# Performance work log

Measured on AMD Instinct MI355X. Metric: run time of the kernel, lower is better.

## Reference

```python
import jax, jax.numpy as jnp
import numpy as np

HID, NH = 2048, 16
QLR, KVLR = 1536, 512
DR, DN, DQK, DV = 64, 128, 192, 128
S = 2048
EPS = 1e-06


def rmsnorm(x, w, eps=EPS):
    return x * jax.lax.rsqrt(jnp.mean(x * x, axis=-1, keepdims=True) + eps) * w


def rope_interleave(x, cos, sin):
    # x: [B,H,S,D]; cos/sin: [B,S,D] (unsqueezed to head dim 1)
    b, h, s, d = x.shape
    # DeepSeek-V3 interleave: (d//2, 2) -> transpose -> flatten
    x = x.reshape(b, h, s, d // 2, 2).swapaxes(3, 4).reshape(b, h, s, d)
    c = cos[:, None, :, :]
    sn = sin[:, None, :, :]
    x1, x2 = x[..., : d // 2], x[..., d // 2:]
    rot = jnp.concatenate([-x2, x1], axis=-1)
    return x * c + rot * sn


def setup_inputs() -> dict:
    key = jax.random.key(0)
    ks = jax.random.split(key, 8)
    hidden_states = jax.random.normal(ks[0], (1, S, HID), dtype=jnp.float32)
    # real RoPE tables for the 64-dim rope part
    inv_freq = 1.0 / (10000.0 ** (np.arange(0, DR, 2, dtype=np.float32) / DR))
    pos = np.arange(S, dtype=np.float32)
    freqs = pos[:, None] * inv_freq[None, :]          # [S, DR/2]
    emb = np.concatenate([freqs, freqs], axis=-1)     # [S, DR]
    cos = jnp.asarray(np.cos(emb), dtype=jnp.float32)[None]
    sin = jnp.asarray(np.sin(emb), dtype=jnp.float32)[None]
    w = 0.02
    wq_a = jax.random.normal(ks[1], (QLR, HID), dtype=jnp.float32) * w
    q_a_ln_w = jnp.ones((QLR,), dtype=jnp.float32)
    wq_b = jax.random.normal(ks[2], (NH * DQK, QLR), dtype=jnp.float32) * w
    wkv_a = jax.random.normal(ks[3], (KVLR + DR, HID), dtype=jnp.float32) * w
    kv_a_ln_w = jnp.ones((KVLR,), dtype=jnp.float32)
    wkv_b = jax.random.normal(ks[4], (NH * (DN + DV), KVLR), dtype=jnp.float32) * w
    wo = jax.random.normal(ks[5], (HID, NH * DV), dtype=jnp.float32) * w
    cu_seqlens = jnp.array([0, S // 2, S], dtype=jnp.int32)  # two packed docs
    return {"hidden_states": hidden_states, "cos": cos, "sin": sin,
            "wq_a": wq_a, "q_a_ln_w": q_a_ln_w, "wq_b": wq_b,
            "wkv_a": wkv_a, "kv_a_ln_w": kv_a_ln_w, "wkv_b": wkv_b,
            "wo": wo, "cu_seqlens": cu_seqlens, "max_seqlen": S // 2}


def reference(hidden_states, cos, sin, wq_a, q_a_ln_w, wq_b, wkv_a, kv_a_ln_w,
              wkv_b, wo, cu_seqlens, max_seqlen):
    B, s, _ = hidden_states.shape
    # LoRA-compressed Q: q_a -> RMSNorm -> q_b
    q = rmsnorm(hidden_states @ wq_a.T, q_a_ln_w) @ wq_b.T       # [B,S,NH*DQK]
    q = q.reshape(B, s, NH, DQK).transpose(0, 2, 1, 3)           # [B,NH,S,DQK]
    q_pass, q_rot = q[..., :DN], q[..., DN:]
    # compressed KV with MQA rope part
    ckv = hidden_states @ wkv_a.T                                 # [B,S,KVLR+DR]
    kv_c, k_rot = ckv[..., :KVLR], ckv[..., KVLR:]
    kv = rmsnorm(kv_c, kv_a_ln_w) @ wkv_b.T                       # [B,S,NH*(DN+DV)]
    kv = kv.reshape(B, s, NH, DN + DV).transpose(0, 2, 1, 3)      # [B,NH,S,DN+DV]
    k_pass, v = kv[..., :DN], kv[..., DN:]
    k_rot = k_rot[:, None, :, :]                                  # [B,1,S,DR]
    q_rot = rope_interleave(q_rot, cos, sin)
    k_rot = rope_interleave(k_rot, cos, sin)
    k_rot = jnp.broadcast_to(k_rot, (B, NH, s, DR))
    qf = jnp.concatenate([q_pass, q_rot], axis=-1)                # [B,NH,S,DQK]
    kf = jnp.concatenate([k_pass, k_rot], axis=-1)                # [B,NH,S,DQK]
    # varlen causal attention: block-diagonal per document + causal
    pos = jnp.arange(s)
    seg = jnp.searchsorted(cu_seqlens[1:], pos, side='right')
    mask = (seg[:, None] == seg[None, :]) & (pos[:, None] >= pos[None, :])
    scale = DQK ** -0.5  # flash default: 1/sqrt(q head dim) (v padded to DQK)
    scores = jnp.einsum('bhqd,bhkd->bhqk', qf, kf) * scale
    scores = jnp.where(mask[None, None], scores, jnp.finfo(scores.dtype).min)
    attn = jax.nn.softmax(scores, axis=-1)
    out = jnp.einsum('bhqk,bhkd->bhqd', attn, v)                  # [B,NH,S,DV]
    out = out.transpose(0, 2, 1, 3).reshape(B, s, NH * DV)
    return out @ wo.T
```

## Files before the change

### kernel.cpp

```cpp
#include <hip/hip_runtime.h>

typedef unsigned short u16;
typedef __attribute__((ext_vector_type(8))) short bf16x8;
typedef __attribute__((ext_vector_type(4))) float f32x4;

#define HID 2048
#define NH 16
#define QLR 1536
#define KVLR 512
#define DR 64
#define DN 128
#define DQK 192
#define DV 128
#define SEQ 2048
#define NKVA 2176
#define SCALE 0.07216878364870323f
#define SCL2 0.1041164359699839f
#define THR2 11.541560327111707f

static __device__ __forceinline__ u16 f2bf(float f) {
  unsigned v = __builtin_bit_cast(unsigned, f);
  v = v + 0x7fffu + ((v >> 16) & 1u);
  return (u16)(v >> 16);
}
static __device__ __forceinline__ float bf2f(u16 u) {
  unsigned v = ((unsigned)u) << 16;
  return __builtin_bit_cast(float, v);
}

#define GLOAD16(gp, lp)                                                        \
  __builtin_amdgcn_global_load_lds(                                            \
      (const __attribute__((address_space(1))) void*)(gp),                     \
      (__attribute__((address_space(3))) void*)(lp), 16, 0, 0)

__global__ void k_convert_all(const float* __restrict__ hs, const float* __restrict__ wq_a,
                              const float* __restrict__ wkv_a, const float* __restrict__ wqb,
                              const float* __restrict__ wkvb, const float* __restrict__ wo,
                              u16* __restrict__ hs_bf, u16* __restrict__ wqkva,
                              u16* __restrict__ wqb_bf, u16* __restrict__ wkvb_bf,
                              u16* __restrict__ wo_bf) {
  const long NQ = 4915200;
  long q = (long)blockIdx.x * blockDim.x + threadIdx.x;
  const long stride = (long)gridDim.x * blockDim.x;
  for (; q < NQ; q += stride) {
    const float* src;
    u16* dst;
    long li;
    bool zero = false;
    if (q < 1048576)        { src = hs;   dst = hs_bf;                      li = q; }
    else if (q < 1835008)   { src = wq_a; dst = wqkva;                      li = q - 1048576; }
    else if (q < 2162688)   { li = q - 1835008; src = wkv_a; dst = wqkva + (size_t)QLR * HID;
                              zero = (li >= 294912); }
    else if (q < 3342336)   { src = wqb;  dst = wqb_bf;                     li = q - 2162688; }
    else if (q < 3866624)   { src = wkvb; dst = wkvb_bf;                    li = q - 3342336; }
    else                    { src = wo;   dst = wo_bf;                      li = q - 3866624; }
    u16 o0 = 0, o1 = 0, o2 = 0, o3 = 0;
    if (!zero) {
      const float4 f = *(const float4*)(src + li * 4);
      o0 = f2bf(f.x); o1 = f2bf(f.y); o2 = f2bf(f.z); o3 = f2bf(f.w);
    }
    u16* d = dst + li * 4;
    d[0] = o0; d[1] = o1; d[2] = o2; d[3] = o3;
  }
}

__global__ void k_rmsnorm2(const float* __restrict__ qkva, const float* __restrict__ qw,
                           const float* __restrict__ kvw, u16* __restrict__ q_ln,
                           u16* __restrict__ kv_ln) {
  const int row = blockIdx.x;
  const int which = blockIdx.y;
  const int t = threadIdx.x;
  const int cols = which ? KVLR : QLR;
  const float inv_cols = which ? (1.0f / KVLR) : (1.0f / QLR);
  const float* x = qkva + (size_t)row * NKVA + (which ? QLR : 0);
  const float* w = which ? kvw : qw;
  u16* Y = (which ? kv_ln : q_ln) + (size_t)row * cols;
  float ss = 0.f;
  for (int i = t * 4; i < cols; i += 1024) {
    float4 v = *(const float4*)(x + i);
    ss += v.x * v.x + v.y * v.y + v.z * v.z + v.w * v.w;
  }
#pragma unroll
  for (int m = 1; m < 64; m <<= 1) ss += __shfl_xor(ss, m, 64);
  __shared__ float red[4];
  if ((t & 63) == 0) red[t >> 6] = ss;
  __syncthreads();
  float tot = red[0] + red[1] + red[2] + red[3];
  float r = rsqrtf(tot * inv_cols + 1e-6f);
  for (int i = t * 4; i < cols; i += 1024) {
    float4 v = *(const float4*)(x + i);
    float4 g = *(const float4*)(w + i);
    u16* y = Y + i;
    y[0] = f2bf(v.x * r * g.x);
    y[1] = f2bf(v.y * r * g.y);
    y[2] = f2bf(v.z * r * g.z);
    y[3] = f2bf(v.w * r * g.w);
  }
}

__global__ __launch_bounds__(256) void k_gemm_nt(
    const u16* __restrict__ A, const u16* __restrict__ B, void* __restrict__ Cout,
    int M, int N, int K, int mode) {
  __shared__ __align__(16) u16 As[2][8192];
  __shared__ __align__(16) u16 Bs[2][8192];
  const int t = threadIdx.x;
  const int lane = t & 63;
  const int w = t >> 6, wr = w >> 1, wc = w & 1;
  const int lm = lane & 15, lg = lane >> 4;

  const int nwg = gridDim.x * gridDim.y;
  int bid = blockIdx.y * gridDim.x + blockIdx.x;
  if ((nwg & 7) == 0) bid = (bid & 7) * (nwg >> 3) + (bid >> 3);
  const int bm = bid % gridDim.y;
  const int bn = bid / gridDim.y;

  const int srow = t >> 3;
  const int scol = ((t & 7) ^ (srow & 7)) * 8;
  const u16* aBase = A + (size_t)(bm * 128 + srow) * K + scol;
  const u16* bBase = B + (size_t)(bn * 128 + srow) * K + scol;
  const size_t rowStep = (size_t)32 * K;

#define STAGE(buf, kt_)                                                        \
  do {                                                                         \
    _Pragma("unroll") for (int p = 0; p < 4; ++p) {                            \
      GLOAD16(aBase + (kt_) + p * rowStep, (u16*)As[buf] + p * 2048 + t * 8);  \
      GLOAD16(bBase + (kt_) + p * rowStep, (u16*)Bs[buf] + p * 2048 + t * 8);  \
    }                                                                          \
  } while (0)

  f32x4 acc[4][4] = {};
  const int nk = K >> 6;
  STAGE(0, 0);
  if (nk > 1) STAGE(1, 64);
  int cur = 0;
  for (int kt = 0; kt < nk; ++kt) {
    if (kt + 1 < nk) asm volatile("s_waitcnt vmcnt(8)" ::: "memory");
    else             asm volatile("s_waitcnt vmcnt(0)" ::: "memory");
    __builtin_amdgcn_s_barrier();
    __builtin_amdgcn_sched_barrier(0);
    bf16x8 af[2][4], bfr[2][4];
#pragma unroll
    for (int kk = 0; kk < 2; ++kk) {
#pragma unroll
      for (int i = 0; i < 4; ++i) {
        const int row_ = wr * 64 + i * 16 + lm;
        af[kk][i] = *(const bf16x8*)(As[cur] + row_ * 64 +
                                     ((((kk << 2) | lg) ^ (row_ & 7)) << 3));
      }
#pragma unroll
      for (int j = 0; j < 4; ++j) {
        const int row_ = wc * 64 + j * 16 + lm;
        bfr[kk][j] = *(const bf16x8*)(Bs[cur] + row_ * 64 +
                                      ((((kk << 2) | lg) ^ (row_ & 7)) << 3));
      }
    }
    asm volatile("s_waitcnt lgkmcnt(0)" ::: "memory");
    __builtin_amdgcn_sched_barrier(0);
    __builtin_amdgcn_s_barrier();
    __builtin_amdgcn_sched_barrier(0);
    if (kt + 2 < nk) STAGE(cur, (kt + 2) << 6);
    __builtin_amdgcn_s_setprio(1);
#pragma unroll
    for (int kk = 0; kk < 2; ++kk)
#pragma unroll
      for (int i = 0; i < 4; ++i)
#pragma unroll
        for (int j = 0; j < 4; ++j)
          acc[i][j] = __builtin_amdgcn_mfma_f32_16x16x32_bf16(af[kk][i], bfr[kk][j],
                                                              acc[i][j], 0, 0, 0);
    __builtin_amdgcn_s_setprio(0);
    cur ^= 1;
  }
#undef STAGE

  const int row0 = bm * 128 + wr * 64 + lg * 4;
  const int col0 = bn * 128 + wc * 64 + lm;
  if (mode == 1) {
    u16* C = (u16*)Cout;
#pragma unroll
    for (int i = 0; i < 4; ++i)
#pragma unroll
      for (int r = 0; r < 4; ++r) {
        u16* crow = C + (size_t)(row0 + i * 16 + r) * N + col0;
#pragma unroll
        for (int j = 0; j < 4; ++j) crow[j * 16] = f2bf(acc[i][j][r]);
      }
  } else {
    float* C = (float*)Cout;
#pragma unroll
    for (int i = 0; i < 4; ++i)
#pragma unroll
      for (int r = 0; r < 4; ++r) {
        float* crow = C + (size_t)(row0 + i * 16 + r) * N + col0;
#pragma unroll
        for (int j = 0; j < 4; ++j) crow[j * 16] = acc[i][j][r];
      }
  }
}

template <int WN>
__global__ __launch_bounds__(512) void k_gemm_nt8(
    const u16* __restrict__ A, const u16* __restrict__ B, void* __restrict__ Cout,
    int M, int N, int K, int mode) {
  constexpr int BN = WN * 64;
  constexpr int NST = 2 + WN;
  __shared__ __align__(16) u16 As[3][128 * 64];
  __shared__ __align__(16) u16 Bs[3][BN * 64];
  const int t = threadIdx.x;
  const int lane = t & 63;
  const int w = t >> 6, wr = w >> 2, wc = w & 3;
  const int lm = lane & 15, lg = lane >> 4;

  const int nwg = gridDim.x * gridDim.y;
  int bid = blockIdx.y * gridDim.x + blockIdx.x;
  if ((nwg & 7) == 0) bid = (bid & 7) * (nwg >> 3) + (bid >> 3);
  const int bm = bid % gridDim.y;
  const int bn = bid / gridDim.y;

  const u16* aT = A + (size_t)bm * 128 * K;
  const u16* bT = B + (size_t)bn * BN * K;

#define STAGE8(buf, kt_)                                                       \
  do {                                                                         \
    _Pragma("unroll") for (int i = 0; i < 2; ++i) {                            \
      const int g = t + i * 512, row = g >> 3, slot = (g & 7) ^ (row & 7);     \
      GLOAD16(aT + (size_t)row * K + slot * 8 + (kt_), (u16*)As[buf] + g * 8); \
    }                                                                          \
    _Pragma("unroll") for (int i = 0; i < WN; ++i) {                           \
      const int g = t + i * 512, row = g >> 3, slot = (g & 7) ^ (row & 7);     \
      GLOAD16(bT + (size_t)row * K + slot * 8 + (kt_), (u16*)Bs[buf] + g * 8); \
    }                                                                          \
  } while (0)

  f32x4 acc[4][WN] = {};
  const int nk = K >> 6;
  STAGE8(0, 0);
  if (nk > 1) STAGE8(1, 64);
  if (nk > 2) STAGE8(2, 128);
  int bt = 0;
  for (int kt = 0; kt < nk; ++kt) {
    const int rem = nk - 1 - kt;
    if (rem >= 2)      asm volatile("s_waitcnt vmcnt(%0)" :: "i"(2 * NST) : "memory");
    else if (rem == 1) asm volatile("s_waitcnt vmcnt(%0)" :: "i"(NST) : "memory");
    else               asm volatile("s_waitcnt vmcnt(0)" ::: "memory");
    __builtin_amdgcn_s_barrier();
    __builtin_amdgcn_sched_barrier(0);
    bf16x8 af[2][4], bfr[2][WN];
#pragma unroll
    for (int kk = 0; kk < 2; ++kk) {
#pragma unroll
      for (int i = 0; i < 4; ++i) {
        const int row_ = wr * 64 + i * 16 + lm;
        af[kk][i] = *(const bf16x8*)(As[bt] + row_ * 64 +
                                     ((((kk << 2) | lg) ^ (row_ & 7)) << 3));
      }
#pragma unroll
      for (int j = 0; j < WN; ++j) {
        const int row_ = wc * (WN * 16) + j * 16 + lm;
        bfr[kk][j] = *(const bf16x8*)(Bs[bt] + row_ * 64 +
                                      ((((kk << 2) | lg) ^ (row_ & 7)) << 3));
      }
    }
    asm volatile("s_waitcnt lgkmcnt(0)" ::: "memory");
    __builtin_amdgcn_sched_barrier(0);
    __builtin_amdgcn_s_barrier();
    __builtin_amdgcn_sched_barrier(0);
    if (kt + 3 < nk) STAGE8(bt, (kt + 3) << 6);
    __builtin_amdgcn_s_setprio(1);
#pragma unroll
    for (int kk = 0; kk < 2; ++kk)
#pragma unroll
      for (int i = 0; i < 4; ++i)
#pragma unroll
        for (int j = 0; j < WN; ++j)
          acc[i][j] = __builtin_amdgcn_mfma_f32_16x16x32_bf16(af[kk][i], bfr[kk][j],
                                                              acc[i][j], 0, 0, 0);
    __builtin_amdgcn_s_setprio(0);
    bt = (bt == 2) ? 0 : bt + 1;
  }
#undef STAGE8

  const int row0 = bm * 128 + wr * 64 + lg * 4;
  const int col0 = bn * BN + wc * (WN * 16) + lm;
  if (mode == 1) {
    u16* C = (u16*)Cout;
#pragma unroll
    for (int i = 0; i < 4; ++i)
#pragma unroll
      for (int r = 0; r < 4; ++r) {
        u16* crow = C + (size_t)(row0 + i * 16 + r) * N + col0;
#pragma unroll
        for (int j = 0; j < WN; ++j) crow[j * 16] = f2bf(acc[i][j][r]);
      }
  } else {
    float* C = (float*)Cout;
#pragma unroll
    for (int i = 0; i < 4; ++i)
#pragma unroll
      for (int r = 0; r < 4; ++r) {
        float* crow = C + (size_t)(row0 + i * 16 + r) * N + col0;
#pragma unroll
        for (int j = 0; j < WN; ++j) crow[j * 16] = acc[i][j][r];
      }
  }
}

__global__ __launch_bounds__(256) void k_mk_all(
    const u16* __restrict__ qfull, const u16* __restrict__ kvfull,
    const float* __restrict__ krot, int krot_stride,
    const float* __restrict__ cosb, const float* __restrict__ sinb,
    u16* __restrict__ qf, u16* __restrict__ kf, u16* __restrict__ vt) {
  __shared__ u16 vts[128][66];
  const int s0 = blockIdx.x * 64, h = blockIdx.y, t = threadIdx.x;
#pragma unroll
  for (int i = 0; i < 8; ++i) {
    const int g = t + i * 256, row = g >> 5, slot = g & 31;
    const u16* src = kvfull + (size_t)(s0 + row) * (NH * 256) + h * 256 + slot * 8;
    bf16x8 v = *(const bf16x8*)src;
    if (slot < 16) {
      *(bf16x8*)(kf + ((size_t)h * SEQ + s0 + row) * DQK + slot * 8) = v;
    } else {
      const int d = (slot - 16) * 8;
#pragma unroll
      for (int e = 0; e < 8; ++e) vts[d + e][row] = (u16)v[e];
    }
  }
#pragma unroll
  for (int i = 0; i < 8; ++i) {
    const int g = t + i * 256, row = g >> 5, c = g & 31;
    float a = krot[(size_t)(s0 + row) * krot_stride + 2 * c];
    float b = krot[(size_t)(s0 + row) * krot_stride + 2 * c + 1];
    float cc = cosb[(size_t)(s0 + row) * DR + c];
    float sn = sinb[(size_t)(s0 + row) * DR + c];
    u16* kd = kf + ((size_t)h * SEQ + s0 + row) * DQK;
    kd[DN + c] = f2bf(a * cc - b * sn);
    kd[DN + 32 + c] = f2bf(b * cc + a * sn);
  }
  __syncthreads();
#pragma unroll
  for (int i = 0; i < 4; ++i) {
    const int g = t + i * 256, d = g >> 3, slot = g & 7;
    bf16x8 v;
#pragma unroll
    for (int e = 0; e < 8; ++e) v[e] = (short)vts[d][slot * 8 + e];
    *(bf16x8*)(vt + ((size_t)h * DV + d) * SEQ + s0 + slot * 8) = v;
  }
#pragma unroll
  for (int i = 0; i < 4; ++i) {
    const int g = t + i * 256, row = g >> 4, vc = g & 15;
    const u16* src = qfull + (size_t)(s0 + row) * (NH * DQK) + h * DQK + vc * 8;
    bf16x8 v = *(const bf16x8*)src;
    bf16x8 o;
#pragma unroll
    for (int e = 0; e < 8; ++e) o[e] = (short)f2bf(bf2f((u16)v[e]) * SCL2);
    *(bf16x8*)(qf + ((size_t)h * SEQ + s0 + row) * DQK + vc * 8) = o;
  }
#pragma unroll
  for (int i = 0; i < 8; ++i) {
    const int g = t + i * 256, row = g >> 5, c = g & 31;
    const u16* src = qfull + (size_t)(s0 + row) * (NH * DQK) + h * DQK;
    float a = bf2f(src[DN + 2 * c]);
    float b = bf2f(src[DN + 2 * c + 1]);
    float cc = cosb[(size_t)(s0 + row) * DR + c];
    float sn = sinb[(size_t)(s0 + row) * DR + c];
    u16* qd = qf + ((size_t)h * SEQ + s0 + row) * DQK;
    qd[DN + c] = f2bf((a * cc - b * sn) * SCL2);
    qd[DN + 32 + c] = f2bf((b * cc + a * sn) * SCL2);
  }
}

__global__ __launch_bounds__(256) void k_attn(
    const u16* __restrict__ qf, const u16* __restrict__ kf, const u16* __restrict__ vt,
    u16* __restrict__ attn_out) {
  __shared__ __align__(16) u16 Ks[3][32 * 192];
  __shared__ __align__(16) u16 Vs[3][128 * 32];
  __shared__ __align__(16) u16 p_lds[4][16][32];

  const int t = threadIdx.x, lane = t & 63, w = t >> 6;
  const int lm = lane & 15, lg = lane >> 4;
  const int bid = blockIdx.x;
  const int x = bid & 7, rr = bid >> 3;
  const int i5 = rr & 31, late = rr >> 5;
  const int tj = late ? (i5 >> 2) : 15 - (i5 >> 2);
  const int h = x * 2 + ((i5 >> 1) & 1);
  const int seg = i5 & 1;
  const int tile_row0 = seg * 1024 + tj * 64;
  const int k_begin = seg * 1024;
  const int n_kt = tj * 2 + 2;

  const int lo_row = tile_row0 + w * 16;
  bf16x8 qfr[6];
  {
    const u16* qp = qf + ((size_t)h * SEQ + (lo_row + lm)) * DQK + lg * 8;
#pragma unroll
    for (int c = 0; c < 6; ++c) qfr[c] = *(const bf16x8*)(qp + c * 32);
  }
  int qrow[4];
#pragma unroll
  for (int r = 0; r < 4; ++r) qrow[r] = lo_row + lg * 4 + r;

  float m_r[4], l_loc[4];
#pragma unroll
  for (int r = 0; r < 4; ++r) { m_r[r] = -3.0e4f; l_loc[r] = 0.f; }
  f32x4 oacc[8] = {};
  bf16x8 pa, vv[8];

#define STAGE(buf, kt_)                                                        \
  do {                                                                         \
    const int k0_ = k_begin + (kt_) * 32;                                      \
    _Pragma("unroll") for (int p = 0; p < 3; ++p) {                            \
      const int id = p * 256 + t;                                              \
      const int row = id / 24, colL = id - row * 24;                           \
      const u16* g = kf + ((size_t)h * SEQ + k0_ + row) * DQK +                \
                     ((colL ^ (row & 7)) * 8);                                 \
      GLOAD16(g, (u16*)Ks[buf] + id * 8);                                      \
    }                                                                          \
    _Pragma("unroll") for (int p = 0; p < 2; ++p) {                            \
      const int id = p * 256 + t;                                              \
      const int row = id >> 2, colL = id & 3;                                  \
      const u16* g = vt + ((size_t)h * DV + row) * SEQ + k0_ +                 \
                     ((colL ^ (row & 3)) * 8);                                 \
      GLOAD16(g, (u16*)Vs[buf] + id * 8);                                      \
    }                                                                          \
  } while (0)

#define COMPUTE1(buf, kt_)                                                     \
  do {                                                                         \
    const int k0_ = k_begin + (kt_) * 32;                                      \
    f32x4 sc[2] = {};                                                          \
    __builtin_amdgcn_s_setprio(1);                                             \
    _Pragma("unroll") for (int n0_ = 0; n0_ < 2; ++n0_)                        \
        _Pragma("unroll") for (int c_ = 0; c_ < 6; ++c_) {                     \
      const int row_ = n0_ * 16 + lm, cc_ = c_ * 4 + lg;                       \
      bf16x8 kfr = *(const bf16x8*)(Ks[buf] + row_ * 192 +                     \
                                    ((cc_ ^ (row_ & 7)) * 8));                 \
      sc[n0_] = __builtin_amdgcn_mfma_f32_16x16x32_bf16(qfr[c_], kfr,          \
                                                        sc[n0_], 0, 0, 0);     \
    }                                                                          \
    __builtin_amdgcn_s_setprio(0);                                             \
    _Pragma("unroll") for (int nd = 0; nd < 8; ++nd) {   \
      const int row_ = nd * 16 + lm;                      \
      vv[nd] = *(const bf16x8*)(Vs[buf] + row_ * 32 +                          \
                                ((lg ^ (row_ & 3)) * 8));                      \
    }                                                                          \
    float s0a[4], s1a[4];                                                      \
    float over = -1e30f;                                                       \
    if (lo_row >= k0_ + 31) {                                                  \
      _Pragma("unroll") for (int r = 0; r < 4; ++r) {                          \
        s0a[r] = sc[0][r];                                                     \
        s1a[r] = sc[1][r];                                                     \
        over = fmaxf(over, fmaxf(s0a[r], s1a[r]) - m_r[r]);                    \
      }                                                                        \
    } else {                                                                   \
      const int kc0 = k0_ + lm, kc1 = k0_ + 16 + lm;                           \
      _Pragma("unroll") for (int r = 0; r < 4; ++r) {                          \
        s0a[r] = (kc0 <= qrow[r]) ? sc[0][r] : -1e30f;                         \
        s1a[r] = (kc1 <= qrow[r]) ? sc[1][r] : -1e30f;                         \
        over = fmaxf(over, fmaxf(s0a[r], s1a[r]) - m_r[r]);                    \
      }                                                                        \
    }                                                                          \
    if (__any(over > THR2)) {                                                  \
      _Pragma("unroll") for (int r = 0; r < 4; ++r) {                          \
        float mx = fmaxf(s0a[r], s1a[r]);                                      \
        _Pragma("unroll") for (int md = 1; md < 16; md <<= 1)                  \
            mx = fmaxf(mx, __shfl_xor(mx, md, 64));                            \
        float mnew = fmaxf(m_r[r], mx);                                        \
        float alpha = exp2f(m_r[r] - mnew);                                    \
        m_r[r] = mnew;                                                         \
        l_loc[r] *= alpha;                                                     \
        _Pragma("unroll") for (int nd = 0; nd < 8; ++nd) oacc[nd][r] *= alpha; \
      }                                                                        \
    }                                                                          \
    _Pragma("unroll") for (int r = 0; r < 4; ++r) {                            \
      float p0 = exp2f(s0a[r] - m_r[r]);                                       \
      float p1 = exp2f(s1a[r] - m_r[r]);                                       \
      l_loc[r] += p0 + p1;                                                     \
      p_lds[w][lg * 4 + r][lm] = f2bf(p0);                                     \
      p_lds[w][lg * 4 + r][16 + lm] = f2bf(p1);                                \
    }                                                                          \
    asm volatile("s_waitcnt lgkmcnt(0)" ::: "memory");                         \
    __builtin_amdgcn_sched_barrier(0);                                         \
    pa = *(const bf16x8*)(&p_lds[w][lm][lg * 8]);                              \
  } while (0)

  STAGE(0, 0);
  STAGE(1, 1);
  if (n_kt > 2) STAGE(2, 2);
  int bt = 0;
  for (int kt = 0; kt < n_kt; ++kt) {
    const int rem = n_kt - 1 - kt;
    if (rem >= 2)      asm volatile("s_waitcnt vmcnt(10)" ::: "memory");
    else if (rem == 1) asm volatile("s_waitcnt vmcnt(5)" ::: "memory");
    else               asm volatile("s_waitcnt vmcnt(0)" ::: "memory");
    __builtin_amdgcn_s_barrier();
    __builtin_amdgcn_sched_barrier(0);
    COMPUTE1(bt, kt);
    asm volatile("s_waitcnt lgkmcnt(0)" ::: "memory");
    __builtin_amdgcn_sched_barrier(0);
    __builtin_amdgcn_s_barrier();
    __builtin_amdgcn_sched_barrier(0);
    if (kt + 3 < n_kt) STAGE(bt, kt + 3);
    __builtin_amdgcn_s_setprio(1);
#pragma unroll
    for (int nd = 0; nd < 8; ++nd)
      oacc[nd] = __builtin_amdgcn_mfma_f32_16x16x32_bf16(pa, vv[nd], oacc[nd], 0, 0, 0);
    __builtin_amdgcn_s_setprio(0);
    bt = (bt == 2) ? 0 : bt + 1;
  }
#undef STAGE
#undef COMPUTE1

#pragma unroll
  for (int r = 0; r < 4; ++r) {
    float lt = l_loc[r];
#pragma unroll
    for (int md = 1; md < 16; md <<= 1) lt += __shfl_xor(lt, md, 64);
    float inv = 1.0f / lt;
#pragma unroll
    for (int nd = 0; nd < 8; ++nd)
      attn_out[(size_t)qrow[r] * (NH * DV) + h * DV + nd * 16 + lm] =
          f2bf(oacc[nd][r] * inv);
  }
}

extern "C" void kernel_launch(void* const* d_in, const int* in_sizes, int n_in,
                              void* d_out, int out_size, void* d_ws, size_t ws_size,
                              hipStream_t stream) {
  const float* hs = (const float*)d_in[0];
  const float* cosb = (const float*)d_in[1];
  const float* sinb = (const float*)d_in[2];
  const float* wq_a = (const float*)d_in[3];
  const float* q_a_ln_w = (const float*)d_in[4];
  const float* wq_b = (const float*)d_in[5];
  const float* wkv_a = (const float*)d_in[6];
  const float* kv_a_ln_w = (const float*)d_in[7];
  const float* wkv_b = (const float*)d_in[8];
  const float* wo = (const float*)d_in[9];

  char* ws = (char*)d_ws;
  size_t off = 0;
  auto take = [&](size_t bytes) {
    size_t o = off;
    off += (bytes + 255) & ~(size_t)255;
    return o;
  };
  u16* hs_bf = (u16*)(ws + take((size_t)SEQ * HID * 2));
  u16* wqkva = (u16*)(ws + take((size_t)NKVA * HID * 2));
  u16* wqb = (u16*)(ws + take((size_t)(NH * DQK) * QLR * 2));
  u16* wkvb = (u16*)(ws + take((size_t)(NH * 256) * KVLR * 2));
  u16* wo_bf = (u16*)(ws + take((size_t)HID * (NH * DV) * 2));
  float* qkva = (float*)(ws + take((size_t)SEQ * NKVA * 4));
  u16* q_ln = (u16*)(ws + take((size_t)SEQ * QLR * 2));
  u16* kv_ln = (u16*)(ws + take((size_t)SEQ * KVLR * 2));
  u16* qfull = (u16*)(ws + take((size_t)SEQ * NH * DQK * 2));
  u16* kvfull = (u16*)(ws + take((size_t)SEQ * NH * 256 * 2));
  u16* qf = (u16*)(ws + take((size_t)NH * SEQ * DQK * 2));
  u16* kf = (u16*)(ws + take((size_t)NH * SEQ * DQK * 2));
  u16* vt = (u16*)(ws + take((size_t)NH * DV * SEQ * 2));
  u16* attn = (u16*)(ws + take((size_t)SEQ * NH * DV * 2));
  if (off > ws_size) return;

  k_convert_all<<<2048, 256, 0, stream>>>(hs, wq_a, wkv_a, wq_b, wkv_b, wo,
                                          hs_bf, wqkva, wqb, wkvb, wo_bf);

  dim3 g1(NKVA / 128, SEQ / 128);
  k_gemm_nt8<2><<<g1, 512, 0, stream>>>(hs_bf, wqkva, qkva, SEQ, NKVA, HID, 0);

  k_rmsnorm2<<<dim3(SEQ, 2), 256, 0, stream>>>(qkva, q_a_ln_w, kv_a_ln_w, q_ln, kv_ln);

  dim3 g2(NH * DQK / 192, SEQ / 128);
  k_gemm_nt8<3><<<g2, 512, 0, stream>>>(q_ln, wqb, qfull, SEQ, NH * DQK, QLR, 1);
  dim3 g3(NH * 256 / 256, SEQ / 128);
  k_gemm_nt8<4><<<g3, 512, 0, stream>>>(kv_ln, wkvb, kvfull, SEQ, NH * 256, KVLR, 1);

  k_mk_all<<<dim3(SEQ / 64, NH), 256, 0, stream>>>(qfull, kvfull, qkva + (QLR + KVLR),
                                                   NKVA, cosb, sinb, qf, kf, vt);

  k_attn<<<512, 256, 0, stream>>>(qf, kf, vt, attn);

  dim3 g4(HID / 128, SEQ / 128);
  k_gemm_nt<<<g4, 256, 0, stream>>>(attn, wo_bf, d_out, SEQ, HID, NH * DV, 0);
}
```

Measured before the change: 201.6 us.

## Split-K the first projection GEMM and fold partial sums into consumers

The q_a/kv_a projection GEMM now runs as a two-way split-K using the 256-thread kernel with a z grid dimension. Each half writes its own fp32 partial buffer, and the RMSNorm and k_rot/RoPE kernels add the two partials when they load them, so no separate reduction kernel is needed. The output projection switches to the 512-thread nt8 kernel with WN=2. This aims to fill more CUs on the small 17x16 tile grid, at the cost of an extra fp32 write and read of the SEQxNKVA intermediate.

New measurement: 187.9 us. -6.8%, faster.

```diff
diff --git a/kernel.cpp b/kernel.cpp
--- a/kernel.cpp
+++ b/kernel.cpp
@@ -64,21 +64,25 @@
   }
 }
 
-__global__ void k_rmsnorm2(const float* __restrict__ qkva, const float* __restrict__ qw,
-                           const float* __restrict__ kvw, u16* __restrict__ q_ln,
-                           u16* __restrict__ kv_ln) {
+__global__ void k_rmsnorm2(const float* __restrict__ qkva0, const float* __restrict__ qkva1,
+                           const float* __restrict__ qw, const float* __restrict__ kvw,
+                           u16* __restrict__ q_ln, u16* __restrict__ kv_ln) {
   const int row = blockIdx.x;
   const int which = blockIdx.y;
   const int t = threadIdx.x;
   const int cols = which ? KVLR : QLR;
   const float inv_cols = which ? (1.0f / KVLR) : (1.0f / QLR);
-  const float* x = qkva + (size_t)row * NKVA + (which ? QLR : 0);
+  const size_t base = (size_t)row * NKVA + (which ? QLR : 0);
+  const float* x0 = qkva0 + base;
+  const float* x1 = qkva1 + base;
   const float* w = which ? kvw : qw;
   u16* Y = (which ? kv_ln : q_ln) + (size_t)row * cols;
   float ss = 0.f;
   for (int i = t * 4; i < cols; i += 1024) {
-    float4 v = *(const float4*)(x + i);
-    ss += v.x * v.x + v.y * v.y + v.z * v.z + v.w * v.w;
+    float4 a = *(const float4*)(x0 + i);
+    float4 b = *(const float4*)(x1 + i);
+    float vx = a.x + b.x, vy = a.y + b.y, vz = a.z + b.z, vw = a.w + b.w;
+    ss += vx * vx + vy * vy + vz * vz + vw * vw;
   }
 #pragma unroll
   for (int m = 1; m < 64; m <<= 1) ss += __shfl_xor(ss, m, 64);
@@ -88,19 +92,20 @@
   float tot = red[0] + red[1] + red[2] + red[3];
   float r = rsqrtf(tot * inv_cols + 1e-6f);
   for (int i = t * 4; i < cols; i += 1024) {
-    float4 v = *(const float4*)(x + i);
+    float4 a = *(const float4*)(x0 + i);
+    float4 b = *(const float4*)(x1 + i);
     float4 g = *(const float4*)(w + i);
     u16* y = Y + i;
-    y[0] = f2bf(v.x * r * g.x);
-    y[1] = f2bf(v.y * r * g.y);
-    y[2] = f2bf(v.z * r * g.z);
-    y[3] = f2bf(v.w * r * g.w);
+    y[0] = f2bf((a.x + b.x) * r * g.x);
+    y[1] = f2bf((a.y + b.y) * r * g.y);
+    y[2] = f2bf((a.z + b.z) * r * g.z);
+    y[3] = f2bf((a.w + b.w) * r * g.w);
   }
 }
 
 __global__ __launch_bounds__(256) void k_gemm_nt(
-    const u16* __restrict__ A, const u16* __restrict__ B, void* __restrict__ Cout,
-    int M, int N, int K, int mode) {
+    const u16* __restrict__ A, const u16* __restrict__ B, float* __restrict__ Cout,
+    int M, int N, int K, int klen) {
   __shared__ __align__(16) u16 As[2][8192];
   __shared__ __align__(16) u16 Bs[2][8192];
   const int t = threadIdx.x;
@@ -113,11 +118,12 @@
   if ((nwg & 7) == 0) bid = (bid & 7) * (nwg >> 3) + (bid >> 3);
   const int bm = bid % gridDim.y;
   const int bn = bid / gridDim.y;
+  const int k0 = blockIdx.z * klen;
 
   const int srow = t >> 3;
   const int scol = ((t & 7) ^ (srow & 7)) * 8;
-  const u16* aBase = A + (size_t)(bm * 128 + srow) * K + scol;
-  const u16* bBase = B + (size_t)(bn * 128 + srow) * K + scol;
+  const u16* aBase = A + (size_t)(bm * 128 + srow) * K + scol + k0;
+  const u16* bBase = B + (size_t)(bn * 128 + srow) * K + scol + k0;
   const size_t rowStep = (size_t)32 * K;
 
 #define STAGE(buf, kt_)                                                        \
@@ -129,7 +135,7 @@
   } while (0)
 
   f32x4 acc[4][4] = {};
-  const int nk = K >> 6;
+  const int nk = klen >> 6;
   STAGE(0, 0);
   if (nk > 1) STAGE(1, 64);
   int cur = 0;
@@ -175,27 +181,15 @@
 
   const int row0 = bm * 128 + wr * 64 + lg * 4;
   const int col0 = bn * 128 + wc * 64 + lm;
-  if (mode == 1) {
-    u16* C = (u16*)Cout;
-#pragma unroll
-    for (int i = 0; i < 4; ++i)
-#pragma unroll
-      for (int r = 0; r < 4; ++r) {
-        u16* crow = C + (size_t)(row0 + i * 16 + r) * N + col0;
-#pragma unroll
-        for (int j = 0; j < 4; ++j) crow[j * 16] = f2bf(acc[i][j][r]);
-      }
-  } else {
-    float* C = (float*)Cout;
-#pragma unroll
-    for (int i = 0; i < 4; ++i)
-#pragma unroll
-      for (int r = 0; r < 4; ++r) {
-        float* crow = C + (size_t)(row0 + i * 16 + r) * N + col0;
-#pragma unroll
-        for (int j = 0; j < 4; ++j) crow[j * 16] = acc[i][j][r];
-      }
-  }
+  float* C = Cout + (size_t)blockIdx.z * M * N;
+#pragma unroll
+  for (int i = 0; i < 4; ++i)
+#pragma unroll
+    for (int r = 0; r < 4; ++r) {
+      float* crow = C + (size_t)(row0 + i * 16 + r) * N + col0;
+#pragma unroll
+      for (int j = 0; j < 4; ++j) crow[j * 16] = acc[i][j][r];
+    }
 }
 
 template <int WN>
@@ -307,7 +301,7 @@
 
 __global__ __launch_bounds__(256) void k_mk_all(
     const u16* __restrict__ qfull, const u16* __restrict__ kvfull,
-    const float* __restrict__ krot, int krot_stride,
+    const float* __restrict__ krot0, const float* __restrict__ krot1, int krot_stride,
     const float* __restrict__ cosb, const float* __restrict__ sinb,
     u16* __restrict__ qf, u16* __restrict__ kf, u16* __restrict__ vt) {
   __shared__ u16 vts[128][66];
@@ -328,8 +322,9 @@
 #pragma unroll
   for (int i = 0; i < 8; ++i) {
     const int g = t + i * 256, row = g >> 5, c = g & 31;
-    float a = krot[(size_t)(s0 + row) * krot_stride + 2 * c];
-    float b = krot[(size_t)(s0 + row) * krot_stride + 2 * c + 1];
+    const size_t kb = (size_t)(s0 + row) * krot_stride + 2 * c;
+    float a = krot0[kb] + krot1[kb];
+    float b = krot0[kb + 1] + krot1[kb + 1];
     float cc = cosb[(size_t)(s0 + row) * DR + c];
     float sn = sinb[(size_t)(s0 + row) * DR + c];
     u16* kd = kf + ((size_t)h * SEQ + s0 + row) * DQK;
@@ -438,8 +433,8 @@
                                                         sc[n0_], 0, 0, 0);     \
     }                                                                          \
     __builtin_amdgcn_s_setprio(0);                                             \
-    _Pragma("unroll") for (int nd = 0; nd < 8; ++nd) {   \
-      const int row_ = nd * 16 + lm;                      \
+    _Pragma("unroll") for (int nd = 0; nd < 8; ++nd) {                         \
+      const int row_ = nd * 16 + lm;                                           \
       vv[nd] = *(const bf16x8*)(Vs[buf] + row_ * 32 +                          \
                                 ((lg ^ (row_ & 3)) * 8));                      \
     }                                                                          \
@@ -549,7 +544,7 @@
   u16* wqb = (u16*)(ws + take((size_t)(NH * DQK) * QLR * 2));
   u16* wkvb = (u16*)(ws + take((size_t)(NH * 256) * KVLR * 2));
   u16* wo_bf = (u16*)(ws + take((size_t)HID * (NH * DV) * 2));
-  float* qkva = (float*)(ws + take((size_t)SEQ * NKVA * 4));
+  float* qkva01 = (float*)(ws + take((size_t)2 * SEQ * NKVA * 4));
   u16* q_ln = (u16*)(ws + take((size_t)SEQ * QLR * 2));
   u16* kv_ln = (u16*)(ws + take((size_t)SEQ * KVLR * 2));
   u16* qfull = (u16*)(ws + take((size_t)SEQ * NH * DQK * 2));
@@ -559,25 +554,29 @@
   u16* vt = (u16*)(ws + take((size_t)NH * DV * SEQ * 2));
   u16* attn = (u16*)(ws + take((size_t)SEQ * NH * DV * 2));
   if (off > ws_size) return;
+  float* qkva0 = qkva01;
+  float* qkva1 = qkva01 + (size_t)SEQ * NKVA;
 
   k_convert_all<<<2048, 256, 0, stream>>>(hs, wq_a, wkv_a, wq_b, wkv_b, wo,
                                           hs_bf, wqkva, wqb, wkvb, wo_bf);
 
-  dim3 g1(NKVA / 128, SEQ / 128);
-  k_gemm_nt8<2><<<g1, 512, 0, stream>>>(hs_bf, wqkva, qkva, SEQ, NKVA, HID, 0);
-
-  k_rmsnorm2<<<dim3(SEQ, 2), 256, 0, stream>>>(qkva, q_a_ln_w, kv_a_ln_w, q_ln, kv_ln);
+  dim3 g1(NKVA / 128, SEQ / 128, 2);
+  k_gemm_nt<<<g1, 256, 0, stream>>>(hs_bf, wqkva, qkva01, SEQ, NKVA, HID, HID / 2);
+
+  k_rmsnorm2<<<dim3(SEQ, 2), 256, 0, stream>>>(qkva0, qkva1, q_a_ln_w, kv_a_ln_w,
+                                               q_ln, kv_ln);
 
   dim3 g2(NH * DQK / 192, SEQ / 128);
   k_gemm_nt8<3><<<g2, 512, 0, stream>>>(q_ln, wqb, qfull, SEQ, NH * DQK, QLR, 1);
   dim3 g3(NH * 256 / 256, SEQ / 128);
   k_gemm_nt8<4><<<g3, 512, 0, stream>>>(kv_ln, wkvb, kvfull, SEQ, NH * 256, KVLR, 1);
 
-  k_mk_all<<<dim3(SEQ / 64, NH), 256, 0, stream>>>(qfull, kvfull, qkva + (QLR + KVLR),
-                                                   NKVA, cosb, sinb, qf, kf, vt);
+  k_mk_all<<<dim3(SEQ / 64, NH), 256, 0, stream>>>(
+      qfull, kvfull, qkva0 + (QLR + KVLR), qkva1 + (QLR + KVLR), NKVA,
+      cosb, sinb, qf, kf, vt);
 
   k_attn<<<512, 256, 0, stream>>>(qf, kf, vt, attn);
 
   dim3 g4(HID / 128, SEQ / 128);
-  k_gemm_nt<<<g4, 256, 0, stream>>>(attn, wo_bf, d_out, SEQ, HID, NH * DV, 0);
-}
+  k_gemm_nt8<2><<<g4, 512, 0, stream>>>(attn, wo_bf, d_out, SEQ, HID, NH * DV, 0);
+}
```

## Split long causal attention tiles across two blocks with merge kernel

Applied to the files above, without the earlier changes.

Attention work for the longer query tiles (tj>=8) is split into two key-range chunks processed by separate workgroups, with partial outputs and softmax stats written to fp32 scratch and combined by a new merge kernel. The grid grows from 512 to 768 blocks, ordered by a static schedule table, and the K/V staging ring drops from three buffers to two. This aims to balance causal-triangle load across CUs at the cost of an extra launch and scratch traffic. It also swaps which GEMM variants handle the first projection and the output projection.

New measurement: 183.0 us. 1.1x faster.

```diff
diff --git a/kernel.cpp b/kernel.cpp
--- a/kernel.cpp
+++ b/kernel.cpp
@@ -99,8 +99,8 @@
 }
 
 __global__ __launch_bounds__(256) void k_gemm_nt(
-    const u16* __restrict__ A, const u16* __restrict__ B, void* __restrict__ Cout,
-    int M, int N, int K, int mode) {
+    const u16* __restrict__ A, const u16* __restrict__ B, float* __restrict__ Cout,
+    int M, int N, int K) {
   __shared__ __align__(16) u16 As[2][8192];
   __shared__ __align__(16) u16 Bs[2][8192];
   const int t = threadIdx.x;
@@ -175,27 +175,14 @@
 
   const int row0 = bm * 128 + wr * 64 + lg * 4;
   const int col0 = bn * 128 + wc * 64 + lm;
-  if (mode == 1) {
-    u16* C = (u16*)Cout;
-#pragma unroll
-    for (int i = 0; i < 4; ++i)
-#pragma unroll
-      for (int r = 0; r < 4; ++r) {
-        u16* crow = C + (size_t)(row0 + i * 16 + r) * N + col0;
-#pragma unroll
-        for (int j = 0; j < 4; ++j) crow[j * 16] = f2bf(acc[i][j][r]);
-      }
-  } else {
-    float* C = (float*)Cout;
-#pragma unroll
-    for (int i = 0; i < 4; ++i)
-#pragma unroll
-      for (int r = 0; r < 4; ++r) {
-        float* crow = C + (size_t)(row0 + i * 16 + r) * N + col0;
-#pragma unroll
-        for (int j = 0; j < 4; ++j) crow[j * 16] = acc[i][j][r];
-      }
-  }
+#pragma unroll
+  for (int i = 0; i < 4; ++i)
+#pragma unroll
+    for (int r = 0; r < 4; ++r) {
+      float* crow = Cout + (size_t)(row0 + i * 16 + r) * N + col0;
+#pragma unroll
+      for (int j = 0; j < 4; ++j) crow[j * 16] = acc[i][j][r];
+    }
 }
 
 template <int WN>
@@ -328,8 +315,9 @@
 #pragma unroll
   for (int i = 0; i < 8; ++i) {
     const int g = t + i * 256, row = g >> 5, c = g & 31;
-    float a = krot[(size_t)(s0 + row) * krot_stride + 2 * c];
-    float b = krot[(size_t)(s0 + row) * krot_stride + 2 * c + 1];
+    const size_t kb = (size_t)(s0 + row) * krot_stride + 2 * c;
+    float a = krot[kb];
+    float b = krot[kb + 1];
     float cc = cosb[(size_t)(s0 + row) * DR + c];
     float sn = sinb[(size_t)(s0 + row) * DR + c];
     u16* kd = kf + ((size_t)h * SEQ + s0 + row) * DQK;
@@ -371,22 +359,30 @@
 
 __global__ __launch_bounds__(256) void k_attn(
     const u16* __restrict__ qf, const u16* __restrict__ kf, const u16* __restrict__ vt,
-    u16* __restrict__ attn_out) {
-  __shared__ __align__(16) u16 Ks[3][32 * 192];
-  __shared__ __align__(16) u16 Vs[3][128 * 32];
+    u16* __restrict__ attn_out, float* __restrict__ O_part, float* __restrict__ mlbuf) {
+  __shared__ __align__(16) u16 Ks[2][32 * 192];
+  __shared__ __align__(16) u16 Vs[2][128 * 32];
   __shared__ __align__(16) u16 p_lds[4][16][32];
+
+  static const signed char TJ[24] = {15,15,7,14,14,13,13,6,12,12,11,11,5,
+                                     10,10,9,9,4,8,8,3,2,1,0};
+  static const signed char CK[24] = {0,1,2,0,1,0,1,2,0,1,0,1,2,
+                                     0,1,0,1,2,0,1,2,2,2,2};
 
   const int t = threadIdx.x, lane = t & 63, w = t >> 6;
   const int lm = lane & 15, lg = lane >> 4;
   const int bid = blockIdx.x;
   const int x = bid & 7, rr = bid >> 3;
-  const int i5 = rr & 31, late = rr >> 5;
-  const int tj = late ? (i5 >> 2) : 15 - (i5 >> 2);
-  const int h = x * 2 + ((i5 >> 1) & 1);
-  const int seg = i5 & 1;
+  const int hh = rr & 1, idx = rr >> 1;
+  const int seg = idx & 1, slot = idx >> 1;
+  const int tj = TJ[slot], ck = CK[slot];
+  const int h = x * 2 + hh;
   const int tile_row0 = seg * 1024 + tj * 64;
   const int k_begin = seg * 1024;
-  const int n_kt = tj * 2 + 2;
+  const int n_all = 2 * tj + 2;
+  const int kt_lo = (ck == 1) ? (tj + 1) : 0;
+  const int kt_hi = (ck == 0) ? (tj + 1) : n_all;
+  const int n_kt = kt_hi - kt_lo;
 
   const int lo_row = tile_row0 + w * 16;
   bf16x8 qfr[6];
@@ -405,7 +401,7 @@
   f32x4 oacc[8] = {};
   bf16x8 pa, vv[8];
 
-#define STAGE(buf, kt_)                                                        \
+#define STAGEA(buf, kt_)                                                       \
   do {                                                                         \
     const int k0_ = k_begin + (kt_) * 32;                                      \
     _Pragma("unroll") for (int p = 0; p < 3; ++p) {                            \
@@ -438,8 +434,8 @@
                                                         sc[n0_], 0, 0, 0);     \
     }                                                                          \
     __builtin_amdgcn_s_setprio(0);                                             \
-    _Pragma("unroll") for (int nd = 0; nd < 8; ++nd) {   \
-      const int row_ = nd * 16 + lm;                      \
+    _Pragma("unroll") for (int nd = 0; nd < 8; ++nd) {                         \
+      const int row_ = nd * 16 + lm;                                           \
       vv[nd] = *(const bf16x8*)(Vs[buf] + row_ * 32 +                          \
                                 ((lg ^ (row_ & 3)) * 8));                      \
     }                                                                          \
@@ -483,43 +479,94 @@
     pa = *(const bf16x8*)(&p_lds[w][lm][lg * 8]);                              \
   } while (0)
 
-  STAGE(0, 0);
-  STAGE(1, 1);
-  if (n_kt > 2) STAGE(2, 2);
-  int bt = 0;
-  for (int kt = 0; kt < n_kt; ++kt) {
-    const int rem = n_kt - 1 - kt;
-    if (rem >= 2)      asm volatile("s_waitcnt vmcnt(10)" ::: "memory");
-    else if (rem == 1) asm volatile("s_waitcnt vmcnt(5)" ::: "memory");
-    else               asm volatile("s_waitcnt vmcnt(0)" ::: "memory");
+  STAGEA(0, kt_lo);
+  STAGEA(1, kt_lo + 1);
+  for (int i = 0; i < n_kt; ++i) {
+    const int kt = kt_lo + i;
+    if (i + 1 < n_kt) asm volatile("s_waitcnt vmcnt(5)" ::: "memory");
+    else              asm volatile("s_waitcnt vmcnt(0)" ::: "memory");
     __builtin_amdgcn_s_barrier();
     __builtin_amdgcn_sched_barrier(0);
-    COMPUTE1(bt, kt);
+    COMPUTE1(i & 1, kt);
     asm volatile("s_waitcnt lgkmcnt(0)" ::: "memory");
     __builtin_amdgcn_sched_barrier(0);
     __builtin_amdgcn_s_barrier();
     __builtin_amdgcn_sched_barrier(0);
-    if (kt + 3 < n_kt) STAGE(bt, kt + 3);
+    if (i + 2 < n_kt) STAGEA(i & 1, kt + 2);
     __builtin_amdgcn_s_setprio(1);
 #pragma unroll
     for (int nd = 0; nd < 8; ++nd)
       oacc[nd] = __builtin_amdgcn_mfma_f32_16x16x32_bf16(pa, vv[nd], oacc[nd], 0, 0, 0);
     __builtin_amdgcn_s_setprio(0);
-    bt = (bt == 2) ? 0 : bt + 1;
-  }
-#undef STAGE
+  }
+#undef STAGEA
 #undef COMPUTE1
 
+  float l_row[4];
 #pragma unroll
   for (int r = 0; r < 4; ++r) {
     float lt = l_loc[r];
 #pragma unroll
     for (int md = 1; md < 16; md <<= 1) lt += __shfl_xor(lt, md, 64);
-    float inv = 1.0f / lt;
-#pragma unroll
-    for (int nd = 0; nd < 8; ++nd)
-      attn_out[(size_t)qrow[r] * (NH * DV) + h * DV + nd * 16 + lm] =
-          f2bf(oacc[nd][r] * inv);
+    l_row[r] = lt;
+  }
+
+  if (ck == 2) {
+#pragma unroll
+    for (int r = 0; r < 4; ++r) {
+      float inv = 1.0f / l_row[r];
+#pragma unroll
+      for (int nd = 0; nd < 8; ++nd)
+        attn_out[(size_t)qrow[r] * (NH * DV) + h * DV + nd * 16 + lm] =
+            f2bf(oacc[nd][r] * inv);
+    }
+  } else {
+    const int part = (((tj - 8) * 2 + seg) * 16 + h) * 2 + ck;
+    float* op = O_part + (size_t)part * 8192;
+#pragma unroll
+    for (int r = 0; r < 4; ++r) {
+      const int rw = w * 16 + lg * 4 + r;
+#pragma unroll
+      for (int nd = 0; nd < 8; ++nd)
+        op[rw * 128 + nd * 16 + lm] = oacc[nd][r];
+      if (lm == 0) {
+        mlbuf[part * 128 + rw] = m_r[r];
+        mlbuf[part * 128 + 64 + rw] = l_row[r];
+      }
+    }
+  }
+}
+
+__global__ __launch_bounds__(256) void k_merge(const float* __restrict__ O_part,
+                                               const float* __restrict__ mlbuf,
+                                               u16* __restrict__ attn_out) {
+  const int b = blockIdx.x;
+  const int h = b & 15, z = b >> 4;
+  const int tj = 8 + (z >> 1), seg = z & 1;
+  const int p0 = (((tj - 8) * 2 + seg) * 16 + h) * 2;
+  const int p1 = p0 + 1;
+  const int t = threadIdx.x;
+  const int row = t >> 2, cg = t & 3;
+
+  const float m0 = mlbuf[p0 * 128 + row], l0 = mlbuf[p0 * 128 + 64 + row];
+  const float m1 = mlbuf[p1 * 128 + row], l1 = mlbuf[p1 * 128 + 64 + row];
+  const float M = fmaxf(m0, m1);
+  const float w0 = exp2f(m0 - M), w1 = exp2f(m1 - M);
+  const float inv = 1.0f / (w0 * l0 + w1 * l1);
+  const float a0 = w0 * inv, a1 = w1 * inv;
+
+  const int qrow = seg * 1024 + tj * 64 + row;
+  const float* o0 = O_part + (size_t)p0 * 8192 + row * 128 + cg * 32;
+  const float* o1 = O_part + (size_t)p1 * 8192 + row * 128 + cg * 32;
+  u16* dst = attn_out + (size_t)qrow * (NH * DV) + h * DV + cg * 32;
+#pragma unroll
+  for (int e = 0; e < 32; e += 4) {
+    const float4 u = *(const float4*)(o0 + e);
+    const float4 v = *(const float4*)(o1 + e);
+    dst[e]     = f2bf(a0 * u.x + a1 * v.x);
+    dst[e + 1] = f2bf(a0 * u.y + a1 * v.y);
+    dst[e + 2] = f2bf(a0 * u.z + a1 * v.z);
+    dst[e + 3] = f2bf(a0 * u.w + a1 * v.w);
   }
 }
 
@@ -559,12 +606,14 @@
   u16* vt = (u16*)(ws + take((size_t)NH * DV * SEQ * 2));
   u16* attn = (u16*)(ws + take((size_t)SEQ * NH * DV * 2));
   if (off > ws_size) return;
+  float* O_part = (float*)kvfull;
+  float* mlbuf = (float*)qfull;
 
   k_convert_all<<<2048, 256, 0, stream>>>(hs, wq_a, wkv_a, wq_b, wkv_b, wo,
                                           hs_bf, wqkva, wqb, wkvb, wo_bf);
 
   dim3 g1(NKVA / 128, SEQ / 128);
-  k_gemm_nt8<2><<<g1, 512, 0, stream>>>(hs_bf, wqkva, qkva, SEQ, NKVA, HID, 0);
+  k_gemm_nt<<<g1, 256, 0, stream>>>(hs_bf, wqkva, qkva, SEQ, NKVA, HID);
 
   k_rmsnorm2<<<dim3(SEQ, 2), 256, 0, stream>>>(qkva, q_a_ln_w, kv_a_ln_w, q_ln, kv_ln);
 
@@ -576,8 +625,9 @@
   k_mk_all<<<dim3(SEQ / 64, NH), 256, 0, stream>>>(qfull, kvfull, qkva + (QLR + KVLR),
                                                    NKVA, cosb, sinb, qf, kf, vt);
 
-  k_attn<<<512, 256, 0, stream>>>(qf, kf, vt, attn);
+  k_attn<<<768, 256, 0, stream>>>(qf, kf, vt, attn, O_part, mlbuf);
+  k_merge<<<256, 256, 0, stream>>>(O_part, mlbuf, attn);
 
   dim3 g4(HID / 128, SEQ / 128);
-  k_gemm_nt<<<g4, 256, 0, stream>>>(attn, wo_bf, d_out, SEQ, HID, NH * DV, 0);
-}
+  k_gemm_nt8<2><<<g4, 512, 0, stream>>>(attn, wo_bf, d_out, SEQ, HID, NH * DV, 0);
+}
```
